# Kernel tuning notes

Measured on AMD Instinct MI355X. Metric: run time of the kernel, lower is better.

## Reference

```python
import jax, jax.numpy as jnp
import numpy as np

HEADS = 8
Q_DIM = 128
V_DIM = 128
OUT_DIM = 128
SCALE = OUT_DIM ** (-0.5)


def _lrelu(x):
    return jnp.where(x >= 0, x, 0.01 * x)


def _gelu(x):
    return jax.nn.gelu(x, approximate=False)


def setup_inputs() -> dict:
    key = jax.random.key(0)
    ks = iter(jax.random.split(key, 32))
    B, H, W, N = 4, 32, 32, 2048
    p = lambda *s: jax.random.normal(next(ks), s, dtype=jnp.float32) * 0.02
    return {
        "query": jax.random.normal(next(ks), (B, Q_DIM, H, W), dtype=jnp.float32),
        "fts": jax.random.normal(next(ks), (B * HEADS, V_DIM, N), dtype=jnp.float32),
        # 1x1 conv proj_q_c: Conv2d(q_dim, q_dim*heads)
        "wqc": p(Q_DIM * HEADS, Q_DIM), "bqc": p(Q_DIM * HEADS),
        # proj_q_l: Linear(q,q) -> LeakyReLU -> Linear(q,out) -> GELU
        "wq1": p(Q_DIM, Q_DIM), "bq1": p(Q_DIM),
        "wq2": p(OUT_DIM, Q_DIM), "bq2": p(OUT_DIM),
        # proj_k
        "wk1": p(V_DIM, V_DIM), "bk1": p(V_DIM),
        "wk2": p(OUT_DIM, V_DIM), "bk2": p(OUT_DIM),
        # proj_v
        "wv1": p(V_DIM, V_DIM), "bv1": p(V_DIM),
        "wv2": p(OUT_DIM, V_DIM), "bv2": p(OUT_DIM),
        # proj_out 1x1 conv (out_dim -> out_dim)
        "wo": p(OUT_DIM, OUT_DIM), "bo": p(OUT_DIM),
        # final_out: Linear(out*heads, out) -> LReLU -> Linear(out,out) -> LReLU
        "wf1": p(OUT_DIM, OUT_DIM * HEADS), "bf1": p(OUT_DIM),
        "wf2": p(OUT_DIM, OUT_DIM), "bf2": p(OUT_DIM),
    }


def reference(query, fts, wqc, bqc, wq1, bq1, wq2, bq2, wk1, bk1, wk2, bk2,
              wv1, bv1, wv2, bv2, wo, bo, wf1, bf1, wf2, bf2):
    B, C, H, W = query.shape
    # 1x1 conv q projection: [B, heads*q_dim, H, W]
    q1 = jnp.einsum('bchw,oc->bohw', query, wqc) + bqc[None, :, None, None]
    # rearrange 'b (h c) l w -> (b h) (l w) c'
    qh = q1.reshape(B, HEADS, C, H, W).transpose(0, 1, 3, 4, 2).reshape(B * HEADS, H * W, C)
    q = _gelu(_lrelu(qh @ wq1.T + bq1) @ wq2.T + bq2)            # [B*h, HW, D]
    ft = fts.transpose(0, 2, 1)                                   # [B*h, N, v_dim]
    k = _gelu(_lrelu(ft @ wk1.T + bk1) @ wk2.T + bk2)             # [B*h, N, D]
    v = _gelu(_lrelu(ft @ wv1.T + bv1) @ wv2.T + bv2)             # [B*h, N, D]
    attn = jax.nn.softmax(jnp.einsum('bmd,bnd->bmn', q, k) * SCALE, axis=-1)
    enh = jnp.einsum('bmn,bnd->bmd', attn, v)                     # [B*h, HW, D]
    enh4 = enh.transpose(0, 2, 1).reshape(B * HEADS, OUT_DIM, H, W)
    ho = jnp.einsum('bdhw,od->bohw', enh4, wo) + bo[None, :, None, None]
    # rearrange '(b h) c l w -> b l w (h c)'
    x = ho.reshape(B, HEADS, OUT_DIM, H, W).transpose(0, 3, 4, 1, 2).reshape(B, H, W, HEADS * OUT_DIM)
    out = _lrelu(_lrelu(x @ wf1.T + bf1) @ wf2.T + bf2)           # [B, H, W, D]
    return out
```

## Files before the change

### kernel.cpp

```cpp
#include <hip/hip_runtime.h>
#include <math.h>

typedef __attribute__((ext_vector_type(8))) __bf16 bf16x8;
typedef __attribute__((ext_vector_type(4))) float f32x4;
typedef __attribute__((ext_vector_type(4))) unsigned u32x4;

__device__ __forceinline__ float act_lrelu(float x) { return x >= 0.0f ? x : 0.01f * x; }
__device__ __forceinline__ float act_gelu(float x) { return 0.5f * x * (1.0f + erff(x * 0.7071067811865475f)); }
__device__ __forceinline__ ushort f2bf(float f) {
    unsigned u = __builtin_bit_cast(unsigned, f);
    u += 0x7fffu + ((u >> 16) & 1u);
    return (ushort)(u >> 16);
}
__device__ __forceinline__ unsigned pack2bf(float lo, float hi) {
    return (unsigned)f2bf(lo) | ((unsigned)f2bf(hi) << 16);
}

__device__ __forceinline__ void stage_wbf(const ushort* __restrict__ Wg,
                                          ushort* Wl, int tid)
{
    #pragma unroll
    for (int it = 0; it < 8; ++it) {
        const int lin = (tid + it * 256) * 8;
        const int r = lin >> 7, c = lin & 127;
        const bf16x8 v = *(const bf16x8*)&Wg[lin];
        *(bf16x8*)&Wl[r * 128 + (c ^ ((r & 7) << 3))] = v;
    }
}

__device__ __forceinline__ void layer8swz(const bf16x8 a[4], const ushort* Wl,
                                          f32x4 acc[8], int l15, int lk8)
{
    const int sx = (l15 & 7) << 3;
    #pragma unroll
    for (int ds = 0; ds < 4; ++ds) {
        const int cb = (ds * 32 + lk8) ^ sx;
        #pragma unroll
        for (int nt = 0; nt < 8; ++nt) {
            const bf16x8 b = *(const bf16x8*)&Wl[(nt * 16 + l15) * 128 + cb];
            acc[nt] = __builtin_amdgcn_mfma_f32_16x16x32_bf16(a[ds], b, acc[nt], 0, 0, 0);
        }
    }
}

template <int ACT>
__device__ __forceinline__ void retile_swz(const f32x4 acc[8], const float bias[8],
                                           ushort* tlw, int l15, int lr4, int lk8,
                                           bf16x8 aout[4])
{
    #pragma unroll
    for (int nt = 0; nt < 8; ++nt)
        #pragma unroll
        for (int j = 0; j < 4; ++j) {
            float v = acc[nt][j] + bias[nt];
            if constexpr (ACT == 1) v = act_lrelu(v);
            if constexpr (ACT == 2) v = act_gelu(v);
            const int row = lr4 + j;
            tlw[row * 128 + ((nt * 16 + l15) ^ ((row & 7) << 3))] = f2bf(v);
        }
    const int sx = (l15 & 7) << 3;
    #pragma unroll
    for (int ds = 0; ds < 4; ++ds)
        aout[ds] = *(const bf16x8*)&tlw[l15 * 128 + ((ds * 32 + lk8) ^ sx)];
}

__device__ __forceinline__ void transpose_tile(
    const float* __restrict__ IN, ushort* __restrict__ OUTb,
    int C, int N, int bx, int by, int bz, float (*T)[68], int tid)
{
    const int r = tid >> 4, c4 = (tid & 15) * 4;
    const int n0 = bx * 64, c0 = by * 64;
    const size_t ib = (size_t)bz * C * N;
    const size_t ob = (size_t)bz * N * C;
    #pragma unroll
    for (int p = 0; p < 4; ++p) {
        const int cl = r + p * 16;
        const float4 v = *(const float4*)&IN[ib + (size_t)(c0 + cl) * N + n0 + c4];
        *(float4*)&T[cl][c4] = v;
    }
    __syncthreads();
    #pragma unroll
    for (int p = 0; p < 4; ++p) {
        const int nl = r + p * 16;
        ushort4 u;
        u.x = f2bf(T[c4 + 0][nl]);
        u.y = f2bf(T[c4 + 1][nl]);
        u.z = f2bf(T[c4 + 2][nl]);
        u.w = f2bf(T[c4 + 3][nl]);
        *(ushort4*)&OUTb[ob + (size_t)(n0 + nl) * C + c0 + c4] = u;
    }
}

__global__ __launch_bounds__(256) void prep_kernel(
    const float* __restrict__ wqc, const float* __restrict__ wq1,
    const float* __restrict__ wq2, const float* __restrict__ wk1,
    const float* __restrict__ wk2, const float* __restrict__ wv1,
    const float* __restrict__ wv2, const float* __restrict__ wf2,
    const float* __restrict__ query, const float* __restrict__ fts,
    const float* __restrict__ wo, const float* __restrict__ wf1,
    const float* __restrict__ bo, const float* __restrict__ bf1,
    ushort* __restrict__ Wdst, ushort* __restrict__ queryT,
    ushort* __restrict__ ftb, ushort* __restrict__ Wcomb,
    float* __restrict__ bconst)
{
    __shared__ __align__(16) char sbuf[32768];
    const int tid = threadIdx.x;
    const int blk = blockIdx.x;

    if (blk < 60) {
        #pragma unroll
        for (int p = 0; p < 4; ++p) {
            const int lin = blk * 4096 + p * 1024 + tid * 4;
            const float* s;
            if (lin < 131072) s = wqc + lin;
            else {
                const int m = (lin - 131072) >> 14, idx = (lin - 131072) & 16383;
                s = (m == 0) ? wq1 + idx : (m == 1) ? wq2 + idx : (m == 2) ? wk1 + idx :
                    (m == 3) ? wk2 + idx : (m == 4) ? wv1 + idx : (m == 5) ? wv2 + idx
                             : wf2 + idx;
            }
            const float4 v = *(const float4*)s;
            ushort4 u; u.x = f2bf(v.x); u.y = f2bf(v.y); u.z = f2bf(v.z); u.w = f2bf(v.w);
            *(ushort4*)&Wdst[lin] = u;
        }
    } else if (blk < 188) {
        const int b2 = blk - 60;
        transpose_tile(query, queryT, 128, 1024, b2 & 15, (b2 >> 4) & 1, b2 >> 5,
                       (float(*)[68])sbuf, tid);
    } else if (blk < 196) {
        ushort* Wl = (ushort*)sbuf;
        const int h = blk - 188;
        const int lane = tid & 63, w = tid >> 6;
        const int l15 = lane & 15, lk8 = (lane >> 4) * 8, lr4 = (lane >> 4) * 4;
        #pragma unroll
        for (int it = 0; it < 16; ++it) {
            const int lin = (tid + it * 256) * 4;
            const int o = lin >> 7, d4 = lin & 127;
            const float4 v = *(const float4*)&wo[o * 128 + d4];
            #pragma unroll
            for (int j = 0; j < 4; ++j) {
                const int d = d4 + j;
                Wl[d * 128 + (o ^ ((d & 7) << 3))] = f2bf((&v.x)[j]);
            }
        }
        __syncthreads();
        const f32x4 z = {0.f, 0.f, 0.f, 0.f};
        #pragma unroll
        for (int rf = 0; rf < 2; ++rf) {
            const int row = w * 32 + rf * 16;
            bf16x8 a[4];
            #pragma unroll
            for (int ds = 0; ds < 4; ++ds) {
                const size_t base = (size_t)(row + l15) * 1024 + h * 128 + ds * 32 + lk8;
                const float4 lo = *(const float4*)&wf1[base];
                const float4 hi = *(const float4*)&wf1[base + 4];
                u32x4 wv;
                wv[0] = pack2bf(lo.x, lo.y); wv[1] = pack2bf(lo.z, lo.w);
                wv[2] = pack2bf(hi.x, hi.y); wv[3] = pack2bf(hi.z, hi.w);
                a[ds] = __builtin_bit_cast(bf16x8, wv);
            }
            f32x4 acc[8];
            #pragma unroll
            for (int i = 0; i < 8; ++i) acc[i] = z;
            layer8swz(a, Wl, acc, l15, lk8);
            #pragma unroll
            for (int nt = 0; nt < 8; ++nt)
                #pragma unroll
                for (int j = 0; j < 4; ++j)
                    Wcomb[h * 16384 + (row + lr4 + j) * 128 + nt * 16 + l15] =
                        f2bf(acc[nt][j]);
        }
    } else if (blk < 200) {
        float* sm = (float*)sbuf;
        const int jl = tid >> 3, part = tid & 7;
        const int j = (blk - 196) * 32 + jl;
        float4 a4 = {0.f, 0.f, 0.f, 0.f};
        #pragma unroll
        for (int kk = 0; kk < 128; kk += 4) {
            const float4 wv = *(const float4*)&wf1[(size_t)j * 1024 + part * 128 + kk];
            const float4 bv = *(const float4*)&bo[kk];
            a4.x += wv.x * bv.x; a4.y += wv.y * bv.y;
            a4.z += wv.z * bv.z; a4.w += wv.w * bv.w;
        }
        sm[tid] = a4.x + a4.y + a4.z + a4.w;
        __syncthreads();
        if (part == 0) {
            float t = bf1[j];
            #pragma unroll
            for (int p2 = 0; p2 < 8; ++p2) t += sm[jl * 8 + p2];
            bconst[j] = t;
        }
    } else {
        const int b2 = blk - 200;
        transpose_tile(fts, ftb, 128, 2048, b2 & 31, (b2 >> 5) & 1, b2 >> 6,
                       (float(*)[68])sbuf, tid);
    }
}

__global__ __launch_bounds__(256) void mlp1v(
    const ushort* __restrict__ X, const ushort* __restrict__ Wbf,
    const float* __restrict__ Bf, ushort* __restrict__ Y)
{
    __shared__ ushort Wl[128 * 128];
    const int tid = threadIdx.x, lane = tid & 63, w = tid >> 6;
    const int l15 = lane & 15, lk8 = (lane >> 4) * 8, lr4 = (lane >> 4) * 4;
    const int head = (blockIdx.x >> 3) & 7;
    stage_wbf(Wbf + head * 16384, Wl, tid);
    float b0[8];
    #pragma unroll
    for (int nt = 0; nt < 8; ++nt) b0[nt] = Bf[head * 128 + nt * 16 + l15];

    const int m0 = blockIdx.x * 128 + w * 32;
    bf16x8 a0[4], a1[4];
    #pragma unroll
    for (int ds = 0; ds < 4; ++ds) {
        int r0 = m0 + l15, r1 = m0 + 16 + l15;
        r0 = (r0 >> 13) * 1024 + (r0 & 1023);
        r1 = (r1 >> 13) * 1024 + (r1 & 1023);
        a0[ds] = *(const bf16x8*)(X + (size_t)r0 * 128 + ds * 32 + lk8);
        a1[ds] = *(const bf16x8*)(X + (size_t)r1 * 128 + ds * 32 + lk8);
    }
    __syncthreads();
    const f32x4 z = {0.f, 0.f, 0.f, 0.f};
    #pragma unroll
    for (int rf = 0; rf < 2; ++rf) {
        f32x4 acc[8];
        #pragma unroll
        for (int i = 0; i < 8; ++i) acc[i] = z;
        layer8swz(rf ? a1 : a0, Wl, acc, l15, lk8);
        const int row = m0 + rf * 16;
        #pragma unroll
        for (int nt = 0; nt < 8; ++nt)
            #pragma unroll
            for (int j = 0; j < 4; ++j)
                Y[(size_t)(row + lr4 + j) * 128 + nt * 16 + l15] = f2bf(acc[nt][j] + b0[nt]);
    }
}

__global__ __launch_bounds__(256) void mlp2dual(
    const ushort* __restrict__ qh, const ushort* __restrict__ ftb,
    const ushort* __restrict__ Wbf,
    const float* __restrict__ bq1, const float* __restrict__ bq2,
    const float* __restrict__ bk1, const float* __restrict__ bk2,
    const float* __restrict__ bv1, const float* __restrict__ bv2,
    ushort* __restrict__ qbuf, ushort* __restrict__ kbuf,
    ushort* __restrict__ vbufT)
{
    __shared__ ushort W1l[128 * 128], W2l[128 * 128];
    __shared__ ushort tl[4][16 * 128];
    const int tid = threadIdx.x, lane = tid & 63, w = tid >> 6;
    const int l15 = lane & 15, lk8 = (lane >> 4) * 8, lr4 = (lane >> 4) * 4;
    const int blk = blockIdx.x;

    const ushort *X, *W1, *W2;
    const float *B1, *B2;
    ushort* Y;
    bool outt = false;
    int t0, nb, ntiles;
    if (blk < 128) {
        X = qh;  W1 = Wbf + 131072; W2 = Wbf + 147456; B1 = bq1; B2 = bq2;
        Y = qbuf;  t0 = blk; nb = 128; ntiles = 256;
    } else if (blk < 384) {
        X = ftb; W1 = Wbf + 163840; W2 = Wbf + 180224; B1 = bk1; B2 = bk2;
        Y = kbuf;  t0 = blk - 128; nb = 256; ntiles = 512;
    } else {
        X = ftb; W1 = Wbf + 196608; W2 = Wbf + 212992; B1 = bv1; B2 = bv2;
        Y = vbufT; t0 = blk - 384; nb = 256; ntiles = 512; outt = true;
    }
    stage_wbf(W1, W1l, tid);
    stage_wbf(W2, W2l, tid);
    float b1[8], b2[8];
    #pragma unroll
    for (int nt = 0; nt < 8; ++nt) { b1[nt] = B1[nt * 16 + l15]; b2[nt] = B2[nt * 16 + l15]; }
    __syncthreads();

    const f32x4 z = {0.f, 0.f, 0.f, 0.f};
    for (int t = t0; t < ntiles; t += nb) {
        const int mw = t * 128 + w * 32;
        bf16x8 a0[4], a1[4];
        #pragma unroll
        for (int ds = 0; ds < 4; ++ds) {
            a0[ds] = *(const bf16x8*)(X + (size_t)(mw + l15) * 128 + ds * 32 + lk8);
            a1[ds] = *(const bf16x8*)(X + (size_t)(mw + 16 + l15) * 128 + ds * 32 + lk8);
        }
        #pragma unroll
        for (int rf = 0; rf < 2; ++rf) {
            const int row = mw + rf * 16;
            f32x4 acc[8];
            #pragma unroll
            for (int i = 0; i < 8; ++i) acc[i] = z;
            layer8swz(rf ? a1 : a0, W1l, acc, l15, lk8);
            bf16x8 a2[4];
            retile_swz<1>(acc, b1, tl[w], l15, lr4, lk8, a2);
            f32x4 acc2[8];
            #pragma unroll
            for (int i = 0; i < 8; ++i) acc2[i] = z;
            layer8swz(a2, W2l, acc2, l15, lk8);
            if (!outt) {
                #pragma unroll
                for (int nt = 0; nt < 8; ++nt)
                    #pragma unroll
                    for (int j = 0; j < 4; ++j)
                        Y[(size_t)(row + lr4 + j) * 128 + nt * 16 + l15] =
                            f2bf(act_gelu(acc2[nt][j] + b2[nt]));
            } else {
                const int R0 = row + lr4;
                const int bh = R0 >> 11, key = R0 & 2047;
                #pragma unroll
                for (int nt = 0; nt < 8; ++nt) {
                    ushort4 pk;
                    #pragma unroll
                    for (int j = 0; j < 4; ++j)
                        (&pk.x)[j] = f2bf(act_gelu(acc2[nt][j] + b2[nt]));
                    *(ushort4*)&Y[((size_t)bh * 128 + nt * 16 + l15) * 2048 + key] = pk;
                }
            }
        }
    }
}

__global__ __launch_bounds__(128) void outpath2(
    const ushort* __restrict__ E, const ushort* __restrict__ Wcomb,
    const float* __restrict__ bconst, const ushort* __restrict__ Wf2bf,
    const float* __restrict__ Bf2, float* __restrict__ OUT)
{
    __shared__ ushort Wc[128 * 128], W2l[128 * 128];
    __shared__ ushort tl[2][16 * 128];
    const int tid = threadIdx.x, lane = tid & 63, w = tid >> 6;
    const int l15 = lane & 15, lk8 = (lane >> 4) * 8, lr4 = (lane >> 4) * 4;
    const int b = blockIdx.x >> 5;
    const int m0 = (blockIdx.x & 31) * 32;

    #pragma unroll
    for (int it = 0; it < 16; ++it) {
        const int lin = (tid + it * 128) * 8;
        const int r = lin >> 7, c = lin & 127;
        *(bf16x8*)&W2l[r * 128 + (c ^ ((r & 7) << 3))] = *(const bf16x8*)&Wf2bf[lin];
    }
    float bc[8], b2[8];
    #pragma unroll
    for (int nt = 0; nt < 8; ++nt) { bc[nt] = bconst[nt * 16 + l15]; b2[nt] = Bf2[nt * 16 + l15]; }

    const f32x4 z = {0.f, 0.f, 0.f, 0.f};
    f32x4 yacc[8];
    #pragma unroll
    for (int i = 0; i < 8; ++i) yacc[i] = z;

    bf16x8 a[4], an[4], wreg[16];
    auto loadE = [&](int h, bf16x8 dst[4]) {
        const size_t er = ((size_t)((b * 8 + h) * 1024) + m0 + w * 16 + l15) * 128;
        #pragma unroll
        for (int ds = 0; ds < 4; ++ds) dst[ds] = *(const bf16x8*)(E + er + ds * 32 + lk8);
    };
    auto wload = [&](int h) {
        #pragma unroll
        for (int it = 0; it < 16; ++it)
            wreg[it] = *(const bf16x8*)&Wcomb[h * 16384 + (tid + it * 128) * 8];
    };
    auto wwrite = [&]() {
        #pragma unroll
        for (int it = 0; it < 16; ++it) {
            const int lin = (tid + it * 128) * 8;
            const int r = lin >> 7, c = lin & 127;
            *(bf16x8*)&Wc[r * 128 + (c ^ ((r & 7) << 3))] = wreg[it];
        }
    };

    wload(0); wwrite();
    loadE(0, a);
    for (int h = 0; h < 8; ++h) {
        if (h < 7) { wload(h + 1); loadE(h + 1, an); }
        __syncthreads();
        layer8swz(a, Wc, yacc, l15, lk8);
        __syncthreads();
        if (h < 7) {
            wwrite();
            #pragma unroll
            for (int ds = 0; ds < 4; ++ds) a[ds] = an[ds];
        }
    }
    bf16x8 a3[4];
    retile_swz<1>(yacc, bc, tl[w], l15, lr4, lk8, a3);
    f32x4 oacc[8];
    #pragma unroll
    for (int i = 0; i < 8; ++i) oacc[i] = z;
    layer8swz(a3, W2l, oacc, l15, lk8);
    #pragma unroll
    for (int nt = 0; nt < 8; ++nt)
        #pragma unroll
        for (int j = 0; j < 4; ++j)
            OUT[((size_t)b * 1024 + m0 + w * 16 + lr4 + j) * 128 + nt * 16 + l15] =
                act_lrelu(oacc[nt][j] + b2[nt]);
}

__global__ __launch_bounds__(256, 3) void flash_attn_bf16(
    const ushort* __restrict__ Q, const ushort* __restrict__ Kx,
    const ushort* __restrict__ Vt, ushort* __restrict__ O)
{
    constexpr float SCALE = 0.08838834764831845f;
    const int bid = blockIdx.x;
    const int bh = (bid & 7) * 4 + ((bid >> 3) & 3);
    const int m0 = (bid >> 5) * 64;
    const int tid = threadIdx.x;
    const int lane = tid & 63, w = tid >> 6;
    const int l15 = lane & 15, g = lane >> 4;
    const int lk8 = g * 8, lr4 = g * 4;
    const int sxk = (l15 & 7) << 3;
    const int sel = g >> 1;
    const int src0 = l15 + ((lane & 16) << 1);

    __shared__ ushort K_lds[2][64 * 128];
    __shared__ ushort V_lds[128 * 64];

    const ushort* Qb = Q + (size_t)bh * 1024 * 128;
    const ushort* Kb = Kx + (size_t)bh * 2048 * 128;
    const ushort* Vb = Vt + (size_t)bh * 128 * 2048;

    bf16x8 qf[4];
    {
        const int row = m0 + w * 16 + l15;
        #pragma unroll
        for (int ds = 0; ds < 4; ++ds)
            qf[ds] = *(const bf16x8*)(Qb + (size_t)row * 128 + ds * 32 + lk8);
    }

    const int kr = tid >> 4, kc = (tid & 15) * 8;
    const int vr = tid >> 3, vc = (tid & 7) * 8;
    bf16x8 kreg[4], vreg[4];
    #pragma unroll
    for (int it = 0; it < 4; ++it) {
        kreg[it] = *(const bf16x8*)(Kb + (size_t)(kr + it * 16) * 128 + kc);
        vreg[it] = *(const bf16x8*)(Vb + (size_t)(vr + it * 32) * 2048 + vc);
    }
    #pragma unroll
    for (int it = 0; it < 4; ++it) {
        const int r = kr + it * 16;
        *(bf16x8*)&K_lds[0][r * 128 + (kc ^ ((r & 7) << 3))] = kreg[it];
        const int rv = vr + it * 32;
        *(bf16x8*)&V_lds[rv * 64 + (vc ^ ((rv & 7) << 3))] = vreg[it];
    }
    __syncthreads();

    f32x4 oacc[8];
    #pragma unroll
    for (int i = 0; i < 8; ++i) oacc[i] = f32x4{0.f, 0.f, 0.f, 0.f};
    float mrun = -1e30f, lrun = 0.f;
    int cur = 0;

    for (int nt = 0; nt < 32; ++nt) {
        if (nt < 31) {
            const int n1 = (nt + 1) * 64;
            #pragma unroll
            for (int it = 0; it < 4; ++it) {
                kreg[it] = *(const bf16x8*)(Kb + (size_t)(n1 + kr + it * 16) * 128 + kc);
                vreg[it] = *(const bf16x8*)(Vb + (size_t)(vr + it * 32) * 2048 + n1 + vc);
            }
        }
        const ushort* Kc = &K_lds[cur][0];

        f32x4 s[4];
        #pragma unroll
        for (int i = 0; i < 4; ++i) s[i] = f32x4{0.f, 0.f, 0.f, 0.f};
        __builtin_amdgcn_s_setprio(1);
        #pragma unroll
        for (int ds = 0; ds < 4; ++ds)
            #pragma unroll
            for (int ct = 0; ct < 4; ++ct) {
                const bf16x8 kf = *(const bf16x8*)
                    &Kc[(ct * 16 + l15) * 128 + ((ds * 32 + lk8) ^ sxk)];
                s[ct] = __builtin_amdgcn_mfma_f32_16x16x32_bf16(kf, qf[ds], s[ct], 0, 0, 0);
            }
        __builtin_amdgcn_s_setprio(0);

        float mx = fmaxf(fmaxf(fmaxf(s[0][0], s[0][1]), fmaxf(s[0][2], s[0][3])),
                         fmaxf(fmaxf(s[1][0], s[1][1]), fmaxf(s[1][2], s[1][3])));
        mx = fmaxf(mx, fmaxf(fmaxf(fmaxf(s[2][0], s[2][1]), fmaxf(s[2][2], s[2][3])),
                             fmaxf(fmaxf(s[3][0], s[3][1]), fmaxf(s[3][2], s[3][3]))));
        mx *= SCALE;
        mx = fmaxf(mx, __shfl_xor(mx, 16));
        mx = fmaxf(mx, __shfl_xor(mx, 32));

        if (!__all((int)(mx <= mrun + 8.f))) {
            const float mnew = fmaxf(mrun, mx);
            const float fsc = __expf(mrun - mnew);
            mrun = mnew;
            lrun *= fsc;
            #pragma unroll
            for (int dt = 0; dt < 8; ++dt)
                #pragma unroll
                for (int j = 0; j < 4; ++j)
                    oacc[dt][j] *= fsc;
        }

        float p[4][4];
        float sum = 0.f;
        #pragma unroll
        for (int ct = 0; ct < 4; ++ct)
            #pragma unroll
            for (int r = 0; r < 4; ++r) {
                const float e = __expf(s[ct][r] * SCALE - mrun);
                p[ct][r] = e;
                sum += e;
            }
        sum += __shfl_xor(sum, 16);
        sum += __shfl_xor(sum, 32);
        lrun += sum;

        unsigned P2[4][2];
        #pragma unroll
        for (int ct = 0; ct < 4; ++ct) {
            P2[ct][0] = pack2bf(p[ct][0], p[ct][1]);
            P2[ct][1] = pack2bf(p[ct][2], p[ct][3]);
        }

        __builtin_amdgcn_s_setprio(1);
        #pragma unroll
        for (int ks = 0; ks < 2; ++ks) {
            u32x4 wv;
            #pragma unroll
            for (int t = 0; t < 4; ++t) {
                const int src = src0 + ((t >> 1) << 4);
                const unsigned wa = __shfl(P2[ks * 2 + 0][t & 1], src);
                const unsigned wb = __shfl(P2[ks * 2 + 1][t & 1], src);
                wv[t] = sel ? wb : wa;
            }
            const bf16x8 pa = __builtin_bit_cast(bf16x8, wv);
            #pragma unroll
            for (int dt = 0; dt < 8; ++dt) {
                const int rv = dt * 16 + l15;
                const bf16x8 vb = *(const bf16x8*)
                    &V_lds[rv * 64 + ((ks * 32 + lk8) ^ sxk)];
                oacc[dt] = __builtin_amdgcn_mfma_f32_16x16x32_bf16(vb, pa, oacc[dt], 0, 0, 0);
            }
        }
        __builtin_amdgcn_s_setprio(0);

        if (nt < 31) {
            __syncthreads();
            const int nxt = cur ^ 1;
            #pragma unroll
            for (int it = 0; it < 4; ++it) {
                const int r = kr + it * 16;
                *(bf16x8*)&K_lds[nxt][r * 128 + (kc ^ ((r & 7) << 3))] = kreg[it];
                const int rv = vr + it * 32;
                *(bf16x8*)&V_lds[rv * 64 + (vc ^ ((rv & 7) << 3))] = vreg[it];
            }
            __syncthreads();
            cur ^= 1;
        }
    }

    ushort* Ob = O + ((size_t)bh * 1024 + m0 + w * 16 + l15) * 128;
    const float inv = 1.0f / lrun;
    #pragma unroll
    for (int dt = 0; dt < 8; ++dt) {
        ushort4 pk;
        #pragma unroll
        for (int r = 0; r < 4; ++r) (&pk.x)[r] = f2bf(oacc[dt][r] * inv);
        *(ushort4*)&Ob[dt * 16 + lr4] = pk;
    }
}

extern "C" void kernel_launch(void* const* d_in, const int* in_sizes, int n_in,
                              void* d_out, int out_size, void* d_ws, size_t ws_size,
                              hipStream_t stream)
{
    (void)in_sizes; (void)n_in; (void)out_size; (void)ws_size;
    const float* query = (const float*)d_in[0];
    const float* fts   = (const float*)d_in[1];
    const float* wqc = (const float*)d_in[2];
    const float* bqc = (const float*)d_in[3];
    const float* wq1 = (const float*)d_in[4];
    const float* bq1 = (const float*)d_in[5];
    const float* wq2 = (const float*)d_in[6];
    const float* bq2 = (const float*)d_in[7];
    const float* wk1 = (const float*)d_in[8];
    const float* bk1 = (const float*)d_in[9];
    const float* wk2 = (const float*)d_in[10];
    const float* bk2 = (const float*)d_in[11];
    const float* wv1 = (const float*)d_in[12];
    const float* bv1 = (const float*)d_in[13];
    const float* wv2 = (const float*)d_in[14];
    const float* bv2 = (const float*)d_in[15];
    const float* wo  = (const float*)d_in[16];
    const float* bo  = (const float*)d_in[17];
    const float* wf1 = (const float*)d_in[18];
    const float* bf1 = (const float*)d_in[19];
    const float* wf2 = (const float*)d_in[20];
    const float* bf2 = (const float*)d_in[21];
    float* out = (float*)d_out;

    char* ws = (char*)d_ws;
    ushort* ftb    = (ushort*)(ws + 0LL);
    ushort* queryT = (ushort*)(ws + 16777216LL);
    ushort* qh     = (ushort*)(ws + 17825792LL);
    ushort* qbuf   = (ushort*)(ws + 26214400LL);
    ushort* kbuf   = (ushort*)(ws + 34603008LL);
    ushort* vbufT  = (ushort*)(ws + 51380224LL);
    ushort* enh    = (ushort*)(ws + 68157440LL);
    ushort* Wbf    = (ushort*)(ws + 76546048LL);
    ushort* Wcomb  = (ushort*)(ws + 77299712LL);
    float*  bconst = (float*) (ws + 77561856LL);

    ushort* wqc_b = Wbf + 0;
    ushort* wf2_b = Wbf + 229376;

    prep_kernel<<<2248, 256, 0, stream>>>(
        wqc, wq1, wq2, wk1, wk2, wv1, wv2, wf2, query, fts, wo, wf1, bo, bf1,
        Wbf, queryT, ftb, Wcomb, bconst);
    mlp1v<<<256, 256, 0, stream>>>(queryT, wqc_b, bqc, qh);
    mlp2dual<<<640, 256, 0, stream>>>(qh, ftb, Wbf, bq1, bq2, bk1, bk2,
                                      bv1, bv2, qbuf, kbuf, vbufT);
    flash_attn_bf16<<<512, 256, 0, stream>>>(qbuf, kbuf, vbufT, enh);
    outpath2<<<128, 128, 0, stream>>>(enh, Wcomb, bconst, wf2_b, bf2, out);
}
```

Before: 191.6 us.

## Swap MFMA operands in MLP2 and retile hidden activations via lane shuffles

Replaces the combined mlp2dual kernel with a templated mlp2swap kernel launched separately for q, k and v. Each block handles one tile. The weights become the A operand of the MFMA so the accumulator comes out transposed. The hidden-layer activations are then re-laid out for the second GEMM with cross-lane shuffles instead of a round trip through shared memory. This removes the LDS retile buffer and its stores and loads, and allows vectorised output stores for q and k. The cost is three kernel launches instead of one, weights restaged per tile with no persistent loop, and scattered 2-byte stores for the transposed v output.

Result: slower. 215.3 us (+12.4%).

```diff
diff --git a/kernel.cpp b/kernel.cpp
--- a/kernel.cpp
+++ b/kernel.cpp
@@ -39,6 +39,21 @@
         for (int nt = 0; nt < 8; ++nt) {
             const bf16x8 b = *(const bf16x8*)&Wl[(nt * 16 + l15) * 128 + cb];
             acc[nt] = __builtin_amdgcn_mfma_f32_16x16x32_bf16(a[ds], b, acc[nt], 0, 0, 0);
+        }
+    }
+}
+
+__device__ __forceinline__ void layer8swap(const bf16x8 a[4], const ushort* Wl,
+                                           f32x4 acc[8], int l15, int lk8)
+{
+    const int sx = (l15 & 7) << 3;
+    #pragma unroll
+    for (int ds = 0; ds < 4; ++ds) {
+        const int cb = (ds * 32 + lk8) ^ sx;
+        #pragma unroll
+        for (int nt = 0; nt < 8; ++nt) {
+            const bf16x8 wf = *(const bf16x8*)&Wl[(nt * 16 + l15) * 128 + cb];
+            acc[nt] = __builtin_amdgcn_mfma_f32_16x16x32_bf16(wf, a[ds], acc[nt], 0, 0, 0);
         }
     }
 }
@@ -237,84 +252,96 @@
     }
 }
 
-__global__ __launch_bounds__(256) void mlp2dual(
-    const ushort* __restrict__ qh, const ushort* __restrict__ ftb,
-    const ushort* __restrict__ Wbf,
-    const float* __restrict__ bq1, const float* __restrict__ bq2,
-    const float* __restrict__ bk1, const float* __restrict__ bk2,
-    const float* __restrict__ bv1, const float* __restrict__ bv2,
-    ushort* __restrict__ qbuf, ushort* __restrict__ kbuf,
-    ushort* __restrict__ vbufT)
+template <bool OUTT>
+__global__ __launch_bounds__(256) void mlp2swap(
+    const ushort* __restrict__ X,
+    const ushort* __restrict__ W1bf, const float* __restrict__ B1,
+    const ushort* __restrict__ W2bf, const float* __restrict__ B2,
+    ushort* __restrict__ Y)
 {
     __shared__ ushort W1l[128 * 128], W2l[128 * 128];
-    __shared__ ushort tl[4][16 * 128];
     const int tid = threadIdx.x, lane = tid & 63, w = tid >> 6;
-    const int l15 = lane & 15, lk8 = (lane >> 4) * 8, lr4 = (lane >> 4) * 4;
-    const int blk = blockIdx.x;
-
-    const ushort *X, *W1, *W2;
-    const float *B1, *B2;
-    ushort* Y;
-    bool outt = false;
-    int t0, nb, ntiles;
-    if (blk < 128) {
-        X = qh;  W1 = Wbf + 131072; W2 = Wbf + 147456; B1 = bq1; B2 = bq2;
-        Y = qbuf;  t0 = blk; nb = 128; ntiles = 256;
-    } else if (blk < 384) {
-        X = ftb; W1 = Wbf + 163840; W2 = Wbf + 180224; B1 = bk1; B2 = bk2;
-        Y = kbuf;  t0 = blk - 128; nb = 256; ntiles = 512;
-    } else {
-        X = ftb; W1 = Wbf + 196608; W2 = Wbf + 212992; B1 = bv1; B2 = bv2;
-        Y = vbufT; t0 = blk - 384; nb = 256; ntiles = 512; outt = true;
-    }
-    stage_wbf(W1, W1l, tid);
-    stage_wbf(W2, W2l, tid);
-    float b1[8], b2[8];
-    #pragma unroll
-    for (int nt = 0; nt < 8; ++nt) { b1[nt] = B1[nt * 16 + l15]; b2[nt] = B2[nt * 16 + l15]; }
+    const int l15 = lane & 15, g = lane >> 4;
+    const int lk8 = g * 8, lr4 = g * 4;
+    const int sel = g >> 1;
+    const int src0 = l15 + ((lane & 16) << 1);
+    stage_wbf(W1bf, W1l, tid);
+    stage_wbf(W2bf, W2l, tid);
+
+    f32x4 b1v[8], b2v[8];
+    #pragma unroll
+    for (int t = 0; t < 8; ++t) {
+        b1v[t] = *(const f32x4*)&B1[t * 16 + lr4];
+        b2v[t] = *(const f32x4*)&B2[t * 16 + lr4];
+    }
+
+    const int m0 = blockIdx.x * 128 + w * 32;
+    bf16x8 a0[4], a1[4];
+    #pragma unroll
+    for (int ds = 0; ds < 4; ++ds) {
+        a0[ds] = *(const bf16x8*)(X + (size_t)(m0 + l15) * 128 + ds * 32 + lk8);
+        a1[ds] = *(const bf16x8*)(X + (size_t)(m0 + 16 + l15) * 128 + ds * 32 + lk8);
+    }
     __syncthreads();
-
     const f32x4 z = {0.f, 0.f, 0.f, 0.f};
-    for (int t = t0; t < ntiles; t += nb) {
-        const int mw = t * 128 + w * 32;
-        bf16x8 a0[4], a1[4];
-        #pragma unroll
-        for (int ds = 0; ds < 4; ++ds) {
-            a0[ds] = *(const bf16x8*)(X + (size_t)(mw + l15) * 128 + ds * 32 + lk8);
-            a1[ds] = *(const bf16x8*)(X + (size_t)(mw + 16 + l15) * 128 + ds * 32 + lk8);
-        }
-        #pragma unroll
-        for (int rf = 0; rf < 2; ++rf) {
-            const int row = mw + rf * 16;
-            f32x4 acc[8];
-            #pragma unroll
-            for (int i = 0; i < 8; ++i) acc[i] = z;
-            layer8swz(rf ? a1 : a0, W1l, acc, l15, lk8);
-            bf16x8 a2[4];
-            retile_swz<1>(acc, b1, tl[w], l15, lr4, lk8, a2);
-            f32x4 acc2[8];
-            #pragma unroll
-            for (int i = 0; i < 8; ++i) acc2[i] = z;
-            layer8swz(a2, W2l, acc2, l15, lk8);
-            if (!outt) {
+    #pragma unroll
+    for (int rf = 0; rf < 2; ++rf) {
+        const int row0 = m0 + rf * 16;
+        f32x4 acc[8];
+        #pragma unroll
+        for (int i = 0; i < 8; ++i) acc[i] = z;
+        layer8swap(rf ? a1 : a0, W1l, acc, l15, lk8);
+        unsigned t2[8][2];
+        #pragma unroll
+        for (int nt = 0; nt < 8; ++nt) {
+            const float v0 = act_lrelu(acc[nt][0] + b1v[nt][0]);
+            const float v1 = act_lrelu(acc[nt][1] + b1v[nt][1]);
+            const float v2 = act_lrelu(acc[nt][2] + b1v[nt][2]);
+            const float v3 = act_lrelu(acc[nt][3] + b1v[nt][3]);
+            t2[nt][0] = pack2bf(v0, v1);
+            t2[nt][1] = pack2bf(v2, v3);
+        }
+        f32x4 acc2[8];
+        #pragma unroll
+        for (int i = 0; i < 8; ++i) acc2[i] = z;
+        const int sx = (l15 & 7) << 3;
+        #pragma unroll
+        for (int ks = 0; ks < 4; ++ks) {
+            u32x4 wv;
+            #pragma unroll
+            for (int t = 0; t < 4; ++t) {
+                const int src = src0 + ((t >> 1) << 4);
+                const unsigned wa = __shfl(t2[ks * 2 + 0][t & 1], src);
+                const unsigned wb = __shfl(t2[ks * 2 + 1][t & 1], src);
+                wv[t] = sel ? wb : wa;
+            }
+            const bf16x8 tf = __builtin_bit_cast(bf16x8, wv);
+            const int cb = (ks * 32 + lk8) ^ sx;
+            #pragma unroll
+            for (int ot = 0; ot < 8; ++ot) {
+                const bf16x8 wf = *(const bf16x8*)&W2l[(ot * 16 + l15) * 128 + cb];
+                acc2[ot] = __builtin_amdgcn_mfma_f32_16x16x32_bf16(wf, tf, acc2[ot], 0, 0, 0);
+            }
+        }
+        if constexpr (!OUTT) {
+            ushort* Yr = Y + (size_t)(row0 + l15) * 128;
+            #pragma unroll
+            for (int ot = 0; ot < 8; ++ot) {
+                ushort4 pk;
                 #pragma unroll
-                for (int nt = 0; nt < 8; ++nt)
-                    #pragma unroll
-                    for (int j = 0; j < 4; ++j)
-                        Y[(size_t)(row + lr4 + j) * 128 + nt * 16 + l15] =
-                            f2bf(act_gelu(acc2[nt][j] + b2[nt]));
-            } else {
-                const int R0 = row + lr4;
-                const int bh = R0 >> 11, key = R0 & 2047;
+                for (int j = 0; j < 4; ++j)
+                    (&pk.x)[j] = f2bf(act_gelu(acc2[ot][j] + b2v[ot][j]));
+                *(ushort4*)&Yr[ot * 16 + lr4] = pk;
+            }
+        } else {
+            const int bh = row0 >> 11, key = (row0 & 2047) + l15;
+            ushort* Yb = Y + ((size_t)bh * 128) * 2048 + key;
+            #pragma unroll
+            for (int ot = 0; ot < 8; ++ot)
                 #pragma unroll
-                for (int nt = 0; nt < 8; ++nt) {
-                    ushort4 pk;
-                    #pragma unroll
-                    for (int j = 0; j < 4; ++j)
-                        (&pk.x)[j] = f2bf(act_gelu(acc2[nt][j] + b2[nt]));
-                    *(ushort4*)&Y[((size_t)bh * 128 + nt * 16 + l15) * 2048 + key] = pk;
-                }
-            }
+                for (int j = 0; j < 4; ++j)
+                    Yb[(size_t)(ot * 16 + lr4 + j) * 2048] =
+                        f2bf(act_gelu(acc2[ot][j] + b2v[ot][j]));
         }
     }
 }
@@ -609,8 +636,9 @@
         wqc, wq1, wq2, wk1, wk2, wv1, wv2, wf2, query, fts, wo, wf1, bo, bf1,
         Wbf, queryT, ftb, Wcomb, bconst);
     mlp1v<<<256, 256, 0, stream>>>(queryT, wqc_b, bqc, qh);
-    mlp2dual<<<640, 256, 0, stream>>>(qh, ftb, Wbf, bq1, bq2, bk1, bk2,
-                                      bv1, bv2, qbuf, kbuf, vbufT);
+    mlp2swap<false><<<256, 256, 0, stream>>>(qh, Wbf + 131072, bq1, Wbf + 147456, bq2, qbuf);
+    mlp2swap<false><<<512, 256, 0, stream>>>(ftb, Wbf + 163840, bk1, Wbf + 180224, bk2, kbuf);
+    mlp2swap<true><<<512, 256, 0, stream>>>(ftb, Wbf + 196608, bv1, Wbf + 212992, bv2, vbufT);
     flash_attn_bf16<<<512, 256, 0, stream>>>(qbuf, kbuf, vbufT, enh);
     outpath2<<<128, 128, 0, stream>>>(enh, Wcomb, bconst, wf2_b, bf2, out);
 }
```
